# Kernel tuning notes

Hardware: AMD Instinct MI355X
Metric: run time of the kernel (lower is better)

Reference implementation:

```python
import jax, jax.numpy as jnp
import numpy as np

SCALING_FACTOR = 1.0


def setup_inputs() -> dict:
    key = jax.random.key(0)
    k1, k2, k3 = jax.random.split(key, 3)
    B, N1, N2, DX, DZ, NT, NK = 4, 64, 64, 2, 128, 2048, 2
    x_grid = jax.random.uniform(k1, (B, N1, N2, DX), dtype=jnp.float32)
    z_grid = jax.random.normal(k2, (B, N1, N2, DZ), dtype=jnp.float32)
    xt = jax.random.uniform(k3, (B, NT, DX), dtype=jnp.float32)
    # Replicates torch init: logspace around log10(init_lengthscale), inverse-softplus
    init_ls = np.logspace(np.log10(0.1) - 0.5, np.log10(0.1) + 0.5, NK).astype(np.float32)
    init_ls = np.tile(init_ls[None, :], (DX, 1))  # (dim, num_kernels)
    lengthscale_param = jnp.asarray(np.log(np.expm1(init_ls)))
    return {"x_grid": x_grid, "z_grid": z_grid, "xt": xt, "lengthscale_param": lengthscale_param}


def reference(x_grid, z_grid, xt, lengthscale_param):
    B = x_grid.shape[0]
    xg = x_grid.reshape(B, -1, x_grid.shape[-1])   # (b, ng, dx)
    zg = z_grid.reshape(B, -1, z_grid.shape[-1])   # (b, ng, dz)
    ls = 1e-5 + jax.nn.softplus(lengthscale_param)  # (dx, nk)
    # EQ/RBF weights: (b, nt, ng, nk)
    diff = (xt[:, :, None, :, None] - xg[:, None, :, :, None]) / ls[None, None, None]
    weights = jnp.exp(-0.5 * jnp.sum(diff * diff, axis=3))
    # weighted smoothing: per-kernel matmul weights @ z_grid, then interleave as (dz nk)
    out = jnp.einsum('btgk,bgz->btzk', weights, zg) / SCALING_FACTOR  # (b, nt, dz, nk)
    return out.reshape(B, xt.shape[1], -1)  # (b, nt, dz*nk), nk fastest like 'b nt (dz nk)'
```

## Files before the change

### kernel.cpp

```cpp
#include <hip/hip_runtime.h>
#include <hip/hip_bf16.h>
#include <cmath>

#define B_   4
#define NT_  2048
#define G_   4096
#define DZ_  128

typedef __attribute__((ext_vector_type(8))) short bf16x8;
typedef __attribute__((ext_vector_type(4))) float f32x4;

__device__ __forceinline__ float softplus_f(float x) {
    return fmaxf(x, 0.0f) + log1pf(expf(-fabsf(x)));
}

__device__ __forceinline__ void gl2lds16(const void* gsrc, void* ldst) {
    __builtin_amdgcn_global_load_lds(
        (const __attribute__((address_space(1))) unsigned int*)gsrc,
        (__attribute__((address_space(3))) unsigned int*)ldst, 16, 0, 0);
}

__global__ __launch_bounds__(256, 1)
void transpose_z(const float* __restrict__ z, unsigned short* __restrict__ zt)
{
    __shared__ unsigned short tile[64][66];
    const int bx = blockIdx.x;
    const int zti = bx & 1;
    const int gt  = (bx >> 1) & 63;
    const int b   = bx >> 7;
    const int g0 = gt * 64, z0 = zti * 64;
    const int tid = threadIdx.x;
    const int zl = tid & 63, gl = tid >> 6;
    #pragma unroll
    for (int i = 0; i < 16; ++i) {
        const int g = gl + i * 4;
        const float v = z[(size_t)(b * G_ + g0 + g) * DZ_ + z0 + zl];
        unsigned int u = __float_as_uint(v);
        u = u + 0x7FFFu + ((u >> 16) & 1u);
        tile[g][zl] = (unsigned short)(u >> 16);
    }
    __syncthreads();
    const int gp = (tid & 31) * 2, zi = tid >> 5;
    const int c  = (g0 + gp) >> 5, gi = gp & 31;
    #pragma unroll
    for (int i = 0; i < 8; ++i) {
        const int zz = zi + i * 8;
        const unsigned int lo = tile[gp][zz], hi = tile[gp + 1][zz];
        *(unsigned int*)(zt + ((size_t)(b * 128 + c) * 128 + z0 + zz) * 32 + gi)
            = lo | (hi << 16);
    }
}

__global__ __launch_bounds__(512, 2)
void setconv_main(const float* __restrict__ xt,
                  const float* __restrict__ xg,
                  const float* __restrict__ lsp,
                  const unsigned short* __restrict__ Zt,
                  float* __restrict__ out)
{
    __shared__ __align__(16) unsigned short lds[32768];

    const int bx = blockIdx.x;
    const int b  = bx & 3;
    const int tt = bx >> 2;
    const int tid  = threadIdx.x;
    const int w    = tid >> 6;
    const int ts   = w >> 2;
    const int p    = w & 3;
    const int lane = tid & 63;
    const int quad = lane >> 4;
    const int l15  = lane & 15;
    const int t0   = tt * 32;

    float c00, c01, c10, c11;
    {
        const float h = -0.72134752f;
        float ls;
        ls = 1e-5f + softplus_f(lsp[0]); c00 = h / (ls * ls);
        ls = 1e-5f + softplus_f(lsp[1]); c01 = h / (ls * ls);
        ls = 1e-5f + softplus_f(lsp[2]); c10 = h / (ls * ls);
        ls = 1e-5f + softplus_f(lsp[3]); c11 = h / (ls * ls);
    }

    const float xt0 = xt[(size_t)(b * NT_ + t0 + ts * 16 + l15) * 2 + 0];
    const float xt1 = xt[(size_t)(b * NT_ + t0 + ts * 16 + l15) * 2 + 1];

    f32x4 acc[2][8];
    #pragma unroll
    for (int k = 0; k < 2; ++k)
        #pragma unroll
        for (int n = 0; n < 8; ++n) acc[k][n] = (f32x4)0.0f;

    unsigned short* const slot0 = lds + p * 8192;
    unsigned short* const slot1 = slot0 + 4096;
    const float* xgq = xg + (size_t)(b * G_ + p * 1024 + quad * 8) * 2;
    const unsigned short* zs = Zt + (size_t)(b * 128 + p * 32) * 4096
                               + ts * 2048 + lane * 8;

    #define STAGE(C, TILE) {                                                   \
        const unsigned short* zc = zs + (size_t)(C) * 4096;                    \
        _Pragma("unroll")                                                      \
        for (int i = 0; i < 4; ++i)                                            \
            gl2lds16(zc + i * 512, (TILE) + ts * 2048 + i * 512);              \
    }

    float4 xv0 = *(const float4*)(xgq + 0);
    float4 xv1 = *(const float4*)(xgq + 4);
    float4 xv2 = *(const float4*)(xgq + 8);
    float4 xv3 = *(const float4*)(xgq + 12);
    STAGE(0, slot0);
    STAGE(1, slot1);

    #define CHUNK_BODY(CH, TILE)                                               \
    {                                                                          \
        const int ch_ = (CH);                                                  \
        float gx[8], gy[8];                                                    \
        gx[0]=xv0.x; gy[0]=xv0.y; gx[1]=xv0.z; gy[1]=xv0.w;                    \
        gx[2]=xv1.x; gy[2]=xv1.y; gx[3]=xv1.z; gy[3]=xv1.w;                    \
        gx[4]=xv2.x; gy[4]=xv2.y; gx[5]=xv2.z; gy[5]=xv2.w;                    \
        gx[6]=xv3.x; gy[6]=xv3.y; gx[7]=xv3.z; gy[7]=xv3.w;                    \
        union { bf16x8 v; unsigned int u[4]; } a0, a1;                         \
        {                                                                      \
            unsigned int w0b[8], w1b[8];                                       \
            _Pragma("unroll")                                                  \
            for (int j = 0; j < 8; ++j) {                                      \
                const float d0 = xt0 - gx[j];                                  \
                const float d1 = xt1 - gy[j];                                  \
                const float q0 = d0 * d0;                                      \
                const float q1 = d1 * d1;                                      \
                const float e0 = fmaf(q1, c10, q0 * c00);                      \
                const float e1 = fmaf(q1, c11, q0 * c01);                      \
                w0b[j] = __float_as_uint(__builtin_amdgcn_exp2f(e0));          \
                w1b[j] = __float_as_uint(__builtin_amdgcn_exp2f(e1));          \
            }                                                                  \
            _Pragma("unroll")                                                  \
            for (int h = 0; h < 4; ++h) {                                      \
                a0.u[h] = __builtin_amdgcn_perm(w0b[2*h+1], w0b[2*h], 0x07060302u); \
                a1.u[h] = __builtin_amdgcn_perm(w1b[2*h+1], w1b[2*h], 0x07060302u); \
            }                                                                  \
        }                                                                      \
            \
        __builtin_amdgcn_s_waitcnt(0x0F78);                      \
        if (ch_ < 31) {                                                        \
            const float* xp = xgq + (ch_ + 1) * 64;                            \
            xv0 = *(const float4*)(xp + 0);                                    \
            xv1 = *(const float4*)(xp + 4);                                    \
            xv2 = *(const float4*)(xp + 8);                                    \
            xv3 = *(const float4*)(xp + 12);                                   \
        }                                                                      \
        __builtin_amdgcn_s_barrier();       \
        _Pragma("unroll")                                                      \
        for (int nt = 0; nt < 8; ++nt) {                                       \
            const bf16x8 bz = *(const bf16x8*)((TILE) + nt * 512 + l15 * 32 + quad * 8); \
            acc[0][nt] = __builtin_amdgcn_mfma_f32_16x16x32_bf16(a0.v, bz, acc[0][nt], 0, 0, 0); \
            acc[1][nt] = __builtin_amdgcn_mfma_f32_16x16x32_bf16(a1.v, bz, acc[1][nt], 0, 0, 0); \
        }                                                                      \
        __builtin_amdgcn_s_waitcnt(0xC07F);                    \
        __builtin_amdgcn_s_barrier();        \
        if (ch_ < 30) STAGE(ch_ + 2, TILE);                                    \
    }

    for (int q = 0; q < 16; ++q) {
        CHUNK_BODY(2 * q,     slot0);
        CHUNK_BODY(2 * q + 1, slot1);
    }
    #undef CHUNK_BODY
    #undef STAGE

    float* const red = (float*)lds;
    #define RED_W(slot) { \
        float* bp = &red[(slot) * 4096 + lane * 4]; \
        _Pragma("unroll") \
        for (int k = 0; k < 2; ++k) \
            _Pragma("unroll") \
            for (int n = 0; n < 8; ++n) \
                *(f32x4*)(bp + (k * 8 + n) * 256) = acc[k][n]; }
    #define RED_A(slot) { \
        const float* bp = &red[(slot) * 4096 + lane * 4]; \
        _Pragma("unroll") \
        for (int k = 0; k < 2; ++k) \
            _Pragma("unroll") \
            for (int n = 0; n < 8; ++n) \
                acc[k][n] += *(const f32x4*)(bp + (k * 8 + n) * 256); }

    __syncthreads();
    if (p >= 2) RED_W(ts * 2 + (p - 2));
    __syncthreads();
    if (p < 2) RED_A(ts * 2 + p);
    __syncthreads();
    if (p == 1) RED_W(ts);
    __syncthreads();
    if (p == 0) {
        RED_A(ts);
        const int tr = t0 + ts * 16 + quad * 4;
        #pragma unroll
        for (int nt = 0; nt < 8; ++nt) {
            float* ob = out + (size_t)(b * NT_ + tr) * (DZ_ * 2) + (nt * 16 + l15) * 2;
            #pragma unroll
            for (int r = 0; r < 4; ++r)
                *(float2*)(ob + (size_t)r * (DZ_ * 2)) =
                    make_float2(acc[0][nt][r], acc[1][nt][r]);
        }
    }
    #undef RED_W
    #undef RED_A
}

extern "C" void kernel_launch(void* const* d_in, const int* in_sizes, int n_in,
                              void* d_out, int out_size, void* d_ws, size_t ws_size,
                              hipStream_t stream)
{
    const float* x_grid = (const float*)d_in[0];
    const float* z_grid = (const float*)d_in[1];
    const float* xt     = (const float*)d_in[2];
    const float* lsp    = (const float*)d_in[3];
    float* out = (float*)d_out;
    unsigned short* Zt = (unsigned short*)d_ws;

    hipLaunchKernelGGL(transpose_z, dim3(512), dim3(256), 0, stream, z_grid, Zt);
    hipLaunchKernelGGL(setconv_main, dim3(256), dim3(512), 0, stream,
                       xt, x_grid, lsp, Zt, out);
}
```

Baseline: 114.5 us.

## Load Z operands directly into registers with double-buffering instead of LDS staging

```diff
diff --git a/kernel.cpp b/kernel.cpp
--- a/kernel.cpp
+++ b/kernel.cpp
@@ -12,12 +12,6 @@
 
 __device__ __forceinline__ float softplus_f(float x) {
     return fmaxf(x, 0.0f) + log1pf(expf(-fabsf(x)));
-}
-
-__device__ __forceinline__ void gl2lds16(const void* gsrc, void* ldst) {
-    __builtin_amdgcn_global_load_lds(
-        (const __attribute__((address_space(1))) unsigned int*)gsrc,
-        (__attribute__((address_space(3))) unsigned int*)ldst, 16, 0, 0);
 }
 
 __global__ __launch_bounds__(256, 1)
@@ -58,7 +52,7 @@
                   const unsigned short* __restrict__ Zt,
                   float* __restrict__ out)
 {
-    __shared__ __align__(16) unsigned short lds[32768];
+    __shared__ __align__(16) float red[16384];
 
     const int bx = blockIdx.x;
     const int b  = bx & 3;
@@ -91,29 +85,24 @@
         #pragma unroll
         for (int n = 0; n < 8; ++n) acc[k][n] = (f32x4)0.0f;
 
-    unsigned short* const slot0 = lds + p * 8192;
-    unsigned short* const slot1 = slot0 + 4096;
+    const unsigned short* zb = Zt + (size_t)(b * 128 + p * 32) * 4096
+                               + l15 * 32 + quad * 8;
     const float* xgq = xg + (size_t)(b * G_ + p * 1024 + quad * 8) * 2;
-    const unsigned short* zs = Zt + (size_t)(b * 128 + p * 32) * 4096
-                               + ts * 2048 + lane * 8;
-
-    #define STAGE(C, TILE) {                                                   \
-        const unsigned short* zc = zs + (size_t)(C) * 4096;                    \
-        _Pragma("unroll")                                                      \
-        for (int i = 0; i < 4; ++i)                                            \
-            gl2lds16(zc + i * 512, (TILE) + ts * 2048 + i * 512);              \
-    }
-
-    float4 xv0 = *(const float4*)(xgq + 0);
-    float4 xv1 = *(const float4*)(xgq + 4);
-    float4 xv2 = *(const float4*)(xgq + 8);
-    float4 xv3 = *(const float4*)(xgq + 12);
-    STAGE(0, slot0);
-    STAGE(1, slot1);
-
-    #define CHUNK_BODY(CH, TILE)                                               \
+
+    bf16x8 bzA[8], bzB[8];
+
+    #pragma unroll
+    for (int nt = 0; nt < 8; ++nt)
+        bzA[nt] = *(const bf16x8*)(zb + nt * 512);
+
+    #define CHUNK(CH, BZC, BZN)                                                \
     {                                                                          \
         const int ch_ = (CH);                                                  \
+        const float* xp = xgq + ch_ * 64;                                      \
+        const float4 xv0 = *(const float4*)(xp + 0);                           \
+        const float4 xv1 = *(const float4*)(xp + 4);                           \
+        const float4 xv2 = *(const float4*)(xp + 8);                           \
+        const float4 xv3 = *(const float4*)(xp + 12);                          \
         float gx[8], gy[8];                                                    \
         gx[0]=xv0.x; gy[0]=xv0.y; gx[1]=xv0.z; gy[1]=xv0.w;                    \
         gx[2]=xv1.x; gy[2]=xv1.y; gx[3]=xv1.z; gy[3]=xv1.w;                    \
@@ -139,35 +128,26 @@
                 a1.u[h] = __builtin_amdgcn_perm(w1b[2*h+1], w1b[2*h], 0x07060302u); \
             }                                                                  \
         }                                                                      \
-            \
-        __builtin_amdgcn_s_waitcnt(0x0F78);                      \
+              \
         if (ch_ < 31) {                                                        \
-            const float* xp = xgq + (ch_ + 1) * 64;                            \
-            xv0 = *(const float4*)(xp + 0);                                    \
-            xv1 = *(const float4*)(xp + 4);                                    \
-            xv2 = *(const float4*)(xp + 8);                                    \
-            xv3 = *(const float4*)(xp + 12);                                   \
+            const unsigned short* zc = zb + (size_t)(ch_ + 1) * 4096;          \
+            _Pragma("unroll")                                                  \
+            for (int nt = 0; nt < 8; ++nt)                                     \
+                BZN[nt] = *(const bf16x8*)(zc + nt * 512);                     \
         }                                                                      \
-        __builtin_amdgcn_s_barrier();       \
         _Pragma("unroll")                                                      \
         for (int nt = 0; nt < 8; ++nt) {                                       \
-            const bf16x8 bz = *(const bf16x8*)((TILE) + nt * 512 + l15 * 32 + quad * 8); \
-            acc[0][nt] = __builtin_amdgcn_mfma_f32_16x16x32_bf16(a0.v, bz, acc[0][nt], 0, 0, 0); \
-            acc[1][nt] = __builtin_amdgcn_mfma_f32_16x16x32_bf16(a1.v, bz, acc[1][nt], 0, 0, 0); \
+            acc[0][nt] = __builtin_amdgcn_mfma_f32_16x16x32_bf16(a0.v, BZC[nt], acc[0][nt], 0, 0, 0); \
+            acc[1][nt] = __builtin_amdgcn_mfma_f32_16x16x32_bf16(a1.v, BZC[nt], acc[1][nt], 0, 0, 0); \
         }                                                                      \
-        __builtin_amdgcn_s_waitcnt(0xC07F);                    \
-        __builtin_amdgcn_s_barrier();        \
-        if (ch_ < 30) STAGE(ch_ + 2, TILE);                                    \
     }
 
     for (int q = 0; q < 16; ++q) {
-        CHUNK_BODY(2 * q,     slot0);
-        CHUNK_BODY(2 * q + 1, slot1);
-    }
-    #undef CHUNK_BODY
-    #undef STAGE
-
-    float* const red = (float*)lds;
+        CHUNK(2 * q,     bzA, bzB);
+        CHUNK(2 * q + 1, bzB, bzA);
+    }
+    #undef CHUNK
+
     #define RED_W(slot) { \
         float* bp = &red[(slot) * 4096 + lane * 4]; \
         _Pragma("unroll") \
```

After: 112.4 us. No clear change (-1.8%).

## Pre-swizzle Z into MFMA fragment layout and restructure chunk pipeline

Applied to the files above, without the earlier changes.

```diff
diff --git a/kernel.cpp b/kernel.cpp
--- a/kernel.cpp
+++ b/kernel.cpp
@@ -8,6 +8,7 @@
 #define DZ_  128
 
 typedef __attribute__((ext_vector_type(8))) short bf16x8;
+typedef __attribute__((ext_vector_type(8))) short s16x8;
 typedef __attribute__((ext_vector_type(4))) float f32x4;
 
 __device__ __forceinline__ float softplus_f(float x) {
@@ -40,14 +41,17 @@
         tile[g][zl] = (unsigned short)(u >> 16);
     }
     __syncthreads();
-    const int gp = (tid & 31) * 2, zi = tid >> 5;
-    const int c  = (g0 + gp) >> 5, gi = gp & 31;
+    const int nt  = tid >> 6;
+    const int q   = (tid >> 4) & 3;
+    const int fl  = tid & 15;
     #pragma unroll
-    for (int i = 0; i < 8; ++i) {
-        const int zz = zi + i * 8;
-        const unsigned int lo = tile[gp][zz], hi = tile[gp + 1][zz];
-        *(unsigned int*)(zt + ((size_t)(b * 128 + c) * 128 + z0 + zz) * 32 + gi)
-            = lo | (hi << 16);
+    for (int i = 0; i < 2; ++i) {
+        s16x8 v;
+        #pragma unroll
+        for (int j = 0; j < 8; ++j)
+            v[j] = (short)tile[i * 32 + q * 8 + j][nt * 16 + fl];
+        *(s16x8*)(zt + ((size_t)(b * 128 + gt * 2 + i) * 8 + zti * 4 + nt) * 512
+                  + (size_t)(q * 16 + fl) * 8) = v;
     }
 }
 
@@ -61,8 +65,8 @@
     __shared__ __align__(16) unsigned short lds[32768];
 
     const int bx = blockIdx.x;
-    const int b  = bx & 3;
-    const int tt = bx >> 2;
+    const int b  = (bx >> 1) & 3;
+    const int tt = ((bx >> 3) << 1) | (bx & 1);
     const int tid  = threadIdx.x;
     const int w    = tid >> 6;
     const int ts   = w >> 2;
@@ -94,38 +98,29 @@
     unsigned short* const slot0 = lds + p * 8192;
     unsigned short* const slot1 = slot0 + 4096;
     const float* xgq = xg + (size_t)(b * G_ + p * 1024 + quad * 8) * 2;
-    const unsigned short* zs = Zt + (size_t)(b * 128 + p * 32) * 4096
-                               + ts * 2048 + lane * 8;
-
-    #define STAGE(C, TILE) {                                                   \
-        const unsigned short* zc = zs + (size_t)(C) * 4096;                    \
+    const unsigned short* zs0 = Zt + (size_t)(b * 128 + p * 32) * 4096 + lane * 8;
+
+    #define STAGE(C, SLOT) {                                                   \
+        const unsigned short* zc = zs0 + (size_t)(C) * 4096;                   \
         _Pragma("unroll")                                                      \
         for (int i = 0; i < 4; ++i)                                            \
-            gl2lds16(zc + i * 512, (TILE) + ts * 2048 + i * 512);              \
-    }
-
-    float4 xv0 = *(const float4*)(xgq + 0);
-    float4 xv1 = *(const float4*)(xgq + 4);
-    float4 xv2 = *(const float4*)(xgq + 8);
-    float4 xv3 = *(const float4*)(xgq + 12);
-    STAGE(0, slot0);
-    STAGE(1, slot1);
-
-    #define CHUNK_BODY(CH, TILE)                                               \
-    {                                                                          \
-        const int ch_ = (CH);                                                  \
-        float gx[8], gy[8];                                                    \
-        gx[0]=xv0.x; gy[0]=xv0.y; gx[1]=xv0.z; gy[1]=xv0.w;                    \
-        gx[2]=xv1.x; gy[2]=xv1.y; gx[3]=xv1.z; gy[3]=xv1.w;                    \
-        gx[4]=xv2.x; gy[4]=xv2.y; gx[5]=xv2.z; gy[5]=xv2.w;                    \
-        gx[6]=xv3.x; gy[6]=xv3.y; gx[7]=xv3.z; gy[7]=xv3.w;                    \
-        union { bf16x8 v; unsigned int u[4]; } a0, a1;                         \
-        {                                                                      \
-            unsigned int w0b[8], w1b[8];                                       \
+            gl2lds16(zc + (ts * 4 + i) * 512, (SLOT) + (ts * 4 + i) * 512);    \
+    }
+
+    union bfu { bf16x8 v; unsigned int u[4]; };
+    bfu aC0, aC1;
+    #define WEIGHTS() {                                                        \
+        _Pragma("unroll")                                                      \
+        for (int jg = 0; jg < 2; ++jg) {                                       \
+            const float4 xa = jg ? xv2 : xv0;                                  \
+            const float4 xb = jg ? xv3 : xv1;                                  \
+            const float px[4] = {xa.x, xa.z, xb.x, xb.z};                      \
+            const float py[4] = {xa.y, xa.w, xb.y, xb.w};                      \
+            unsigned int w0b[4], w1b[4];                                       \
             _Pragma("unroll")                                                  \
-            for (int j = 0; j < 8; ++j) {                                      \
-                const float d0 = xt0 - gx[j];                                  \
-                const float d1 = xt1 - gy[j];                                  \
+            for (int j = 0; j < 4; ++j) {                                      \
+                const float d0 = xt0 - px[j];                                  \
+                const float d1 = xt1 - py[j];                                  \
                 const float q0 = d0 * d0;                                      \
                 const float q1 = d1 * d1;                                      \
                 const float e0 = fmaf(q1, c10, q0 * c00);                      \
@@ -133,38 +128,47 @@
                 w0b[j] = __float_as_uint(__builtin_amdgcn_exp2f(e0));          \
                 w1b[j] = __float_as_uint(__builtin_amdgcn_exp2f(e1));          \
             }                                                                  \
-            _Pragma("unroll")                                                  \
-            for (int h = 0; h < 4; ++h) {                                      \
-                a0.u[h] = __builtin_amdgcn_perm(w0b[2*h+1], w0b[2*h], 0x07060302u); \
-                a1.u[h] = __builtin_amdgcn_perm(w1b[2*h+1], w1b[2*h], 0x07060302u); \
-            }                                                                  \
+            aC0.u[jg * 2 + 0] = __builtin_amdgcn_perm(w0b[1], w0b[0], 0x07060302u); \
+            aC0.u[jg * 2 + 1] = __builtin_amdgcn_perm(w0b[3], w0b[2], 0x07060302u); \
+            aC1.u[jg * 2 + 0] = __builtin_amdgcn_perm(w1b[1], w1b[0], 0x07060302u); \
+            aC1.u[jg * 2 + 1] = __builtin_amdgcn_perm(w1b[3], w1b[2], 0x07060302u); \
         }                                                                      \
-            \
-        __builtin_amdgcn_s_waitcnt(0x0F78);                      \
-        if (ch_ < 31) {                                                        \
-            const float* xp = xgq + (ch_ + 1) * 64;                            \
-            xv0 = *(const float4*)(xp + 0);                                    \
-            xv1 = *(const float4*)(xp + 4);                                    \
-            xv2 = *(const float4*)(xp + 8);                                    \
-            xv3 = *(const float4*)(xp + 12);                                   \
-        }                                                                      \
-        __builtin_amdgcn_s_barrier();       \
-        _Pragma("unroll")                                                      \
-        for (int nt = 0; nt < 8; ++nt) {                                       \
-            const bf16x8 bz = *(const bf16x8*)((TILE) + nt * 512 + l15 * 32 + quad * 8); \
-            acc[0][nt] = __builtin_amdgcn_mfma_f32_16x16x32_bf16(a0.v, bz, acc[0][nt], 0, 0, 0); \
-            acc[1][nt] = __builtin_amdgcn_mfma_f32_16x16x32_bf16(a1.v, bz, acc[1][nt], 0, 0, 0); \
-        }                                                                      \
-        __builtin_amdgcn_s_waitcnt(0xC07F);                    \
-        __builtin_amdgcn_s_barrier();        \
-        if (ch_ < 30) STAGE(ch_ + 2, TILE);                                    \
-    }
-
-    for (int q = 0; q < 16; ++q) {
-        CHUNK_BODY(2 * q,     slot0);
-        CHUNK_BODY(2 * q + 1, slot1);
-    }
-    #undef CHUNK_BODY
+    }
+
+    float4 xv0 = *(const float4*)(xgq + 0);
+    float4 xv1 = *(const float4*)(xgq + 4);
+    float4 xv2 = *(const float4*)(xgq + 8);
+    float4 xv3 = *(const float4*)(xgq + 12);
+    STAGE(0, slot0);
+    WEIGHTS();
+
+    for (int ch = 0; ch < 32; ++ch) {
+        __builtin_amdgcn_s_waitcnt(0x0F70);
+        __builtin_amdgcn_s_barrier();
+
+        if (ch < 31) {
+            const float* xp = xgq + (ch + 1) * 64;
+            xv0 = *(const float4*)(xp + 0);
+            xv1 = *(const float4*)(xp + 4);
+            xv2 = *(const float4*)(xp + 8);
+            xv3 = *(const float4*)(xp + 12);
+            unsigned short* dst = ((ch + 1) & 1) ? slot1 : slot0;
+            STAGE(ch + 1, dst);
+        }
+
+        const unsigned short* tile = (ch & 1) ? slot1 : slot0;
+        __builtin_amdgcn_s_setprio(1);
+        #pragma unroll
+        for (int nt = 0; nt < 8; ++nt) {
+            const bf16x8 bz = *(const bf16x8*)(tile + nt * 512 + lane * 8);
+            acc[0][nt] = __builtin_amdgcn_mfma_f32_16x16x32_bf16(aC0.v, bz, acc[0][nt], 0, 0, 0);
+            acc[1][nt] = __builtin_amdgcn_mfma_f32_16x16x32_bf16(aC1.v, bz, acc[1][nt], 0, 0, 0);
+        }
+        __builtin_amdgcn_s_setprio(0);
+
+        if (ch < 31) WEIGHTS();
+    }
+    #undef WEIGHTS
     #undef STAGE
 
     float* const red = (float*)lds;
```

Measured after the change: 106.3 us. -7.1%, faster.
